# Performance work log

Hardware: AMD Instinct MI355X
Metric: run time of the kernel (lower is better)

The kernel has to match this reference:

```python
import jax, jax.numpy as jnp
import numpy as np

B, LP, LQ, D, H = 4, 256, 256, 256, 256


def setup_inputs() -> dict:
    key = jax.random.key(0)
    ks = jax.random.split(key, 10)
    s_d = 1.0 / np.sqrt(D)
    s_h = 1.0 / np.sqrt(H)
    return {
        "Hp": jax.random.normal(ks[0], (B, LP, D), jnp.float32),
        "Hq": jax.random.normal(ks[1], (B, LQ, D), jnp.float32),
        # weights stored as (in, out); torch Linear does x @ W.T
        "Wc1": jax.random.normal(ks[2], (D, H), jnp.float32) * s_d,
        "Wc2": jax.random.normal(ks[3], (D, H), jnp.float32) * s_d,
        "vc": jax.random.normal(ks[4], (H,), jnp.float32) * s_h,
        "Wb": jax.random.normal(ks[5], (D, D), jnp.float32) * s_d,
        "Wd": jax.random.normal(ks[6], (D, H), jnp.float32) * s_d,
        "vd": jax.random.normal(ks[7], (H,), jnp.float32) * s_h,
        "Wm": jax.random.normal(ks[8], (D, H), jnp.float32) * s_d,
        "vm": jax.random.normal(ks[9], (H,), jnp.float32) * s_h,
    }


def _attend(scores, Hq):
    # scores: (B, Lp, Lq); softmax over Lq then weighted sum of Hq
    a = jax.nn.softmax(scores, axis=2)
    return jnp.einsum("bpq,bqd->bpd", a, Hq)


def reference(Hp, Hq, Wc1, Wc2, vc, Wb, Wd, vd, Wm, vm):
    # branch c: additive attention. tanh(Wc1 Hq + Wc2 Hp) . vc
    s1 = Hq @ Wc1                      # (B, Lq, H)
    s2 = Hp @ Wc2                      # (B, Lp, H)
    sc = jnp.einsum("bpqh,h->bpq", jnp.tanh(s1[:, None, :, :] + s2[:, :, None, :]), vc)
    qc = _attend(sc, Hq)

    # branch b: bilinear attention Hp (Wb Hq)^T
    sb = jnp.einsum("bpd,bqd->bpq", Hp, Hq @ Wb)
    qb = _attend(sb, Hq)

    # branch d: multiplicative interaction. tanh(Wd (Hq * Hp)) . vd
    sd = jnp.einsum("bpqh,h->bpq",
                    jnp.tanh(jnp.einsum("bqk,bpk,kh->bpqh", Hq, Hp, Wd)), vd)
    qd = _attend(sd, Hq)

    # branch m: subtractive interaction. tanh(Wm (Hq - Hp)) . vm
    m1 = Hq @ Wm                       # (B, Lq, H)
    m2 = Hp @ Wm                       # (B, Lp, H)
    sm = jnp.einsum("bpqh,h->bpq", jnp.tanh(m1[:, None, :, :] - m2[:, :, None, :]), vm)
    qm = _attend(sm, Hq)

    return (qc, qb, qd, qm)
```

## Files before the change

kernel.cpp:

```cpp
#include <hip/hip_runtime.h>

#define LOG2E 1.4426950408889634f
#define TANH_S 2.8853900817779268f
#define NB 4
#define NL 256
#define ND 256
#define NH 256

typedef __attribute__((ext_vector_type(8))) short s16x8;
typedef __attribute__((ext_vector_type(4))) short s16x4;
typedef __attribute__((ext_vector_type(4))) float f32x4;
typedef __attribute__((ext_vector_type(2))) unsigned int u32x2;

static __device__ __forceinline__ float b2f(unsigned short u) {
  return __builtin_bit_cast(float, (unsigned int)u << 16);
}
static __device__ __forceinline__ unsigned short f2b(float f) {
  unsigned int x = __builtin_bit_cast(unsigned int, f);
  return (unsigned short)((x + 0x7fffu + ((x >> 16) & 1u)) >> 16);
}
static __device__ __forceinline__ unsigned int cvtpk(float lo, float hi) {
  unsigned int r;
  asm("v_cvt_pk_bf16_f32 %0, %1, %2" : "=v"(r) : "v"(lo), "v"(hi));
  return r;
}


__global__ void __launch_bounds__(256) prep(
    const float* __restrict__ Hq, const float* __restrict__ Hp,
    const float* __restrict__ Wc1, const float* __restrict__ Wc2,
    const float* __restrict__ Wb, const float* __restrict__ Wm,
    const float* __restrict__ Wd, float* __restrict__ ws)
{
  const int which = blockIdx.y;
  const int tid = threadIdx.x;
  __shared__ __align__(16) float a_s[8][256];
  if (which == 5) {
    const int m0 = blockIdx.x * 8;
    unsigned short* AF = (unsigned short*)((char*)ws + 3145728);
    const int row = m0 + (tid >> 5);
    const int grp = tid & 31;
    const int kt = grp >> 2, quad = grp & 3;
    const int k0 = kt * 32 + quad * 8;
    const int bb = row >> 8, q = row & 255;
    const int w = q >> 6, mt = (q >> 4) & 3, c16 = q & 15;
    const float* src = Hq + row * ND + k0;
    f32x4 v0 = *(const f32x4*)(src);
    f32x4 v1 = *(const f32x4*)(src + 4);
    s16x8 o;
    #pragma unroll
    for (int j = 0; j < 4; ++j) { o[j] = (short)f2b(v0[j]); o[4 + j] = (short)f2b(v1[j]); }
    *(s16x8*)(AF + ((((bb * 4 + w) * 4 + mt) * 8 + kt) * 64 + quad * 16 + c16) * 8) = o;
    return;
  }
  if (which == 6) {
    if (blockIdx.x >= 32) return;
    const int k0 = blockIdx.x * 8;
    #pragma unroll
    for (int kk = 0; kk < 8; ++kk)
      a_s[kk][tid] = Wd[(k0 + kk) * NH + tid] * TANH_S;
    __syncthreads();
    float* WdT = (float*)((char*)ws + 4718592);
    f32x4 v0 = {a_s[0][tid], a_s[1][tid], a_s[2][tid], a_s[3][tid]};
    f32x4 v1 = {a_s[4][tid], a_s[5][tid], a_s[6][tid], a_s[7][tid]};
    *(f32x4*)(WdT + tid * 256 + k0) = v0;
    *(f32x4*)(WdT + tid * 256 + k0 + 4) = v1;
    return;
  }
  const int m0 = blockIdx.x * 8;
  const float* A = (which >= 3) ? Hp : Hq;
  const float* W = (which == 0) ? Wc1 : (which == 1) ? Wm :
                   (which == 2) ? Wb  : (which == 3) ? Wc2 : Wm;
  #pragma unroll
  for (int j = 0; j < 8; ++j)
    a_s[j][tid] = A[(m0 + j) * ND + tid];
  __syncthreads();
  float acc[8] = {0.f, 0.f, 0.f, 0.f, 0.f, 0.f, 0.f, 0.f};
  for (int k = 0; k < 256; ++k) {
    const float w = W[k * NH + tid];
    #pragma unroll
    for (int j = 0; j < 8; ++j) acc[j] += a_s[j][k] * w;
  }
  if (which == 2) {
    #pragma unroll
    for (int j = 0; j < 8; ++j) ws[(m0 + j) * NH + tid] = acc[j];
  } else if (which < 2) {
    unsigned short* O = (unsigned short*)((char*)ws + 1048576 + which * 524288);
    #pragma unroll
    for (int j = 0; j < 8; ++j) O[(m0 + j) * NH + tid] = f2b(acc[j] * TANH_S);
  } else {
    unsigned short* O = (unsigned short*)((char*)ws + 2097152 + (which - 3) * 524288);
    #pragma unroll
    for (int j = 0; j < 8; ++j) O[(m0 + j) * NH + tid] = f2b(acc[j] * TANH_S);
  }
}

__global__ void __launch_bounds__(256) dfused(
    const float* __restrict__ Hp, const float* __restrict__ Hq,
    const float* __restrict__ vd, const float* __restrict__ vc,
    const float* __restrict__ vm, const float* __restrict__ ws,
    float* __restrict__ out)
{
  const int p = blockIdx.x, b = blockIdx.y;
  const int tid = threadIdx.x;
  const int wave = tid >> 6, lane = tid & 63;
  const int quad = lane >> 4, c16 = lane & 15;

  __shared__ __align__(16) char ovl[33792];
  __shared__ __align__(16) float sc4[4 * 256];
  __shared__ __align__(16) float hp_s[256];
  __shared__ __align__(16) float invsum[4];

  short* Bs = (short*)ovl;
  float* vd2_s = (float*)(ovl + 32768);
  float* redp = (float*)ovl;
  float* c2_s = (float*)(ovl + 16384);
  float* m2_s = (float*)(ovl + 17408);
  float* vc2_s = (float*)(ovl + 18432);
  float* vm2_s = (float*)(ovl + 19456);

  const unsigned short* AF = (const unsigned short*)((const char*)ws + 3145728);
  const float* WdT = (const float*)((const char*)ws + 4718592);
  const float* X = ws;
  const unsigned short* C1  = (const unsigned short*)((const char*)ws + 1048576);
  const unsigned short* M1  = (const unsigned short*)((const char*)ws + 1572864);
  const unsigned short* C2b = (const unsigned short*)((const char*)ws + 2097152);
  const unsigned short* M2b = (const unsigned short*)((const char*)ws + 2621440);

  hp_s[tid] = Hp[(b * NL + p) * ND + tid];
  vd2_s[tid] = 2.0f * vd[tid];
  __syncthreads();

  {
    const int scol = (tid & 63) * 4;
    const f32x4 hpv = *(const f32x4*)(hp_s + scol);
    const int wq0 = wave * 64;
    const unsigned short* AFw = AF + (b * 4 + wave) * 4 * 8 * 64 * 8;
    const int xswz = (c16 & 7) * 16;

    float sdp[4][4];
    #pragma unroll
    for (int mt = 0; mt < 4; ++mt)
      #pragma unroll
      for (int r = 0; r < 4; ++r) sdp[mt][r] = 0.f;
    float vs2 = 0.f;

    for (int ht = 0; ht < 4; ++ht) {
      const int h0 = ht * 64;
      __syncthreads();
      {
        const float* wsrc = WdT + h0 * 256 + tid * 4;
        #pragma unroll
        for (int i = 0; i < 16; ++i) {
          f32x4 wv = *(const f32x4*)(wsrc + i * 1024);
          const int h = i * 4 + (tid >> 6);
          const unsigned int u0 = cvtpk(wv[0] * hpv[0], wv[1] * hpv[1]);
          const unsigned int u1 = cvtpk(wv[2] * hpv[2], wv[3] * hpv[3]);
          const int baddr = h * 512 + (((tid & 63) * 8) ^ ((h & 7) * 16));
          *(u32x2*)((char*)Bs + baddr) = u32x2{u0, u1};
        }
      }
      __syncthreads();

      f32x4 acc[4][4];
      #pragma unroll
      for (int mt = 0; mt < 4; ++mt)
        #pragma unroll
        for (int nt = 0; nt < 4; ++nt) acc[mt][nt] = f32x4{0.f, 0.f, 0.f, 0.f};

      #pragma unroll 2
      for (int kt = 0; kt < 8; ++kt) {
        s16x8 a8[4];
        #pragma unroll
        for (int mt = 0; mt < 4; ++mt)
          a8[mt] = *(const s16x8*)(AFw + ((mt * 8 + kt) * 64 + lane) * 8);
        #pragma unroll
        for (int nt = 0; nt < 4; ++nt) {
          const int baddr = (nt * 16 + c16) * 512 + ((kt * 64 + quad * 16) ^ xswz);
          s16x8 b8 = *(const s16x8*)((const char*)Bs + baddr);
          #pragma unroll
          for (int mt = 0; mt < 4; ++mt)
            acc[mt][nt] = __builtin_amdgcn_mfma_f32_16x16x32_bf16(
                a8[mt], b8, acc[mt][nt], 0, 0, 0);
        }
      }

      #pragma unroll
      for (int nt = 0; nt < 4; ++nt) {
        const float v2 = vd2_s[h0 + nt * 16 + c16];
        vs2 += v2;
        #pragma unroll
        for (int mt = 0; mt < 4; ++mt) {
          #pragma unroll
          for (int r = 0; r < 4; ++r) {
            float e = __builtin_amdgcn_exp2f(acc[mt][nt][r]);
            sdp[mt][r] += v2 * __builtin_amdgcn_rcpf(e + 1.0f);
          }
        }
      }
    }

    #pragma unroll
    for (int m = 1; m < 16; m <<= 1) vs2 += __shfl_xor(vs2, m, 64);
    #pragma unroll
    for (int mt = 0; mt < 4; ++mt)
      #pragma unroll
      for (int r = 0; r < 4; ++r) {
        float v = sdp[mt][r];
        #pragma unroll
        for (int m = 1; m < 16; m <<= 1) v += __shfl_xor(v, m, 64);
        if (c16 == 0)
          sc4[512 + wq0 + mt * 16 + quad * 4 + r] = 0.5f * vs2 - v;
      }
  }
  __syncthreads();

  {
    const int r = (b * NL + p) * ND + tid;
    c2_s[tid] = b2f(C2b[r]);
    m2_s[tid] = b2f(M2b[r]);
    vc2_s[tid] = 2.0f * vc[tid];
    vm2_s[tid] = 2.0f * vm[tid];
  }
  __syncthreads();

  {
    const int qsub = lane >> 4;
    const int hb = c16 * 4;
    float lc = 0.f, lm = 0.f;
    #pragma unroll
    for (int hi = 0; hi < 4; ++hi) {
      const int h = hb + hi * 64;
      #pragma unroll
      for (int i = 0; i < 4; ++i) { lc += vc2_s[h + i]; lm += vm2_s[h + i]; }
    }
    #pragma unroll
    for (int m = 1; m < 16; m <<= 1) {
      lc += __shfl_xor(lc, m, 64);
      lm += __shfl_xor(lm, m, 64);
    }
    const float c0 = 0.5f * lc, m0 = 0.5f * lm;

    for (int qg = 0; qg < 16; ++qg) {
      const int q = wave * 64 + qg * 4 + qsub;
      const unsigned short* c1r = C1 + (b * NL + q) * NH;
      const unsigned short* m1r = M1 + (b * NL + q) * NH;
      const float* xr = X + (b * NL + q) * ND;
      float pcr0 = 0.f, pmr0 = 0.f, pb0 = 0.f;
      float pcr1 = 0.f, pmr1 = 0.f, pb1 = 0.f;
      #pragma unroll
      for (int hi = 0; hi < 4; ++hi) {
        const int h = hb + hi * 64;
        s16x4 c1v = *(const s16x4*)(c1r + h);
        s16x4 m1v = *(const s16x4*)(m1r + h);
        f32x4 xv  = *(const f32x4*)(xr + h);
        #pragma unroll
        for (int i = 0; i < 4; ++i) {
          float ec = __builtin_amdgcn_exp2f(b2f((unsigned short)c1v[i]) + c2_s[h + i]);
          float em = __builtin_amdgcn_exp2f(b2f((unsigned short)m1v[i]) - m2_s[h + i]);
          if (i & 1) {
            pcr1 += vc2_s[h + i] * __builtin_amdgcn_rcpf(ec + 1.0f);
            pmr1 += vm2_s[h + i] * __builtin_amdgcn_rcpf(em + 1.0f);
            pb1 += hp_s[h + i] * xv[i];
          } else {
            pcr0 += vc2_s[h + i] * __builtin_amdgcn_rcpf(ec + 1.0f);
            pmr0 += vm2_s[h + i] * __builtin_amdgcn_rcpf(em + 1.0f);
            pb0 += hp_s[h + i] * xv[i];
          }
        }
      }
      float pcr = pcr0 + pcr1, pmr = pmr0 + pmr1, pb = pb0 + pb1;
      #pragma unroll
      for (int m = 1; m < 16; m <<= 1) {
        pcr += __shfl_xor(pcr, m, 64);
        pmr += __shfl_xor(pmr, m, 64);
        pb  += __shfl_xor(pb, m, 64);
      }
      if (c16 == 0) {
        sc4[q]       = c0 - pcr;
        sc4[256 + q] = pb;
        sc4[768 + q] = m0 - pmr;
      }
    }
  }
  __syncthreads();

  {
    float s0 = sc4[wave * 256 + lane];
    float s1 = sc4[wave * 256 + lane + 64];
    float s2 = sc4[wave * 256 + lane + 128];
    float s3 = sc4[wave * 256 + lane + 192];
    float mx = fmaxf(fmaxf(s0, s1), fmaxf(s2, s3));
    #pragma unroll
    for (int m = 1; m < 64; m <<= 1) mx = fmaxf(mx, __shfl_xor(mx, m, 64));
    float e0 = __builtin_amdgcn_exp2f((s0 - mx) * LOG2E);
    float e1 = __builtin_amdgcn_exp2f((s1 - mx) * LOG2E);
    float e2 = __builtin_amdgcn_exp2f((s2 - mx) * LOG2E);
    float e3 = __builtin_amdgcn_exp2f((s3 - mx) * LOG2E);
    float sm = e0 + e1 + e2 + e3;
    #pragma unroll
    for (int m = 1; m < 64; m <<= 1) sm += __shfl_xor(sm, m, 64);
    sc4[wave * 256 + lane]       = e0;
    sc4[wave * 256 + lane + 64]  = e1;
    sc4[wave * 256 + lane + 128] = e2;
    sc4[wave * 256 + lane + 192] = e3;
    if (lane == 0) invsum[wave] = __builtin_amdgcn_rcpf(sm);
  }
  __syncthreads();

  {
    const int q0 = wave * 64;
    f32x4 pa0 = {0.f,0.f,0.f,0.f}, pa1 = {0.f,0.f,0.f,0.f};
    f32x4 pa2 = {0.f,0.f,0.f,0.f}, pa3 = {0.f,0.f,0.f,0.f};
    for (int qi = 0; qi < 64; ++qi) {
      const int q = q0 + qi;
      const float ac = sc4[q];
      const float ab = sc4[256 + q];
      const float ad = sc4[512 + q];
      const float am = sc4[768 + q];
      f32x4 hv = *(const f32x4*)(Hq + (b * NL + q) * ND + lane * 4);
      pa0 += ac * hv; pa1 += ab * hv; pa2 += ad * hv; pa3 += am * hv;
    }
    *(f32x4*)(redp + (wave * 4 + 0) * 256 + lane * 4) = pa0;
    *(f32x4*)(redp + (wave * 4 + 1) * 256 + lane * 4) = pa1;
    *(f32x4*)(redp + (wave * 4 + 2) * 256 + lane * 4) = pa2;
    *(f32x4*)(redp + (wave * 4 + 3) * 256 + lane * 4) = pa3;
  }
  __syncthreads();

  {
    #pragma unroll
    for (int br = 0; br < 4; ++br) {
      float s = redp[(0 * 4 + br) * 256 + tid] + redp[(1 * 4 + br) * 256 + tid]
              + redp[(2 * 4 + br) * 256 + tid] + redp[(3 * 4 + br) * 256 + tid];
      out[((br * NB + b) * NL + p) * ND + tid] = s * invsum[br];
    }
  }
}

extern "C" void kernel_launch(void* const* d_in, const int* in_sizes, int n_in,
                              void* d_out, int out_size, void* d_ws, size_t ws_size,
                              hipStream_t stream) {
  const float* Hp  = (const float*)d_in[0];
  const float* Hq  = (const float*)d_in[1];
  const float* Wc1 = (const float*)d_in[2];
  const float* Wc2 = (const float*)d_in[3];
  const float* vc  = (const float*)d_in[4];
  const float* Wb  = (const float*)d_in[5];
  const float* Wd  = (const float*)d_in[6];
  const float* vd  = (const float*)d_in[7];
  const float* Wm  = (const float*)d_in[8];
  const float* vm  = (const float*)d_in[9];
  float* ws = (float*)d_ws;
  float* out = (float*)d_out;

  hipLaunchKernelGGL(prep, dim3(128, 7), dim3(256), 0, stream,
                     Hq, Hp, Wc1, Wc2, Wb, Wm, Wd, ws);
  hipLaunchKernelGGL(dfused, dim3(256, 4), dim3(256), 0, stream,
                     Hp, Hq, vd, vc, vm, ws, out);
}
```

Before: 198.5 us.

## Move projection GEMMs to split-bf16 MFMA kernel with pre-transposed weights

```diff
diff --git a/kernel.cpp b/kernel.cpp
--- a/kernel.cpp
+++ b/kernel.cpp
@@ -27,7 +27,7 @@
 
 
 __global__ void __launch_bounds__(256) prep(
-    const float* __restrict__ Hq, const float* __restrict__ Hp,
+    const float* __restrict__ Hq,
     const float* __restrict__ Wc1, const float* __restrict__ Wc2,
     const float* __restrict__ Wb, const float* __restrict__ Wm,
     const float* __restrict__ Wd, float* __restrict__ ws)
@@ -35,7 +35,7 @@
   const int which = blockIdx.y;
   const int tid = threadIdx.x;
   __shared__ __align__(16) float a_s[8][256];
-  if (which == 5) {
+  if (which == 0) {
     const int m0 = blockIdx.x * 8;
     unsigned short* AF = (unsigned short*)((char*)ws + 3145728);
     const int row = m0 + (tid >> 5);
@@ -53,7 +53,7 @@
     *(s16x8*)(AF + ((((bb * 4 + w) * 4 + mt) * 8 + kt) * 64 + quad * 16 + c16) * 8) = o;
     return;
   }
-  if (which == 6) {
+  if (which == 1) {
     if (blockIdx.x >= 32) return;
     const int k0 = blockIdx.x * 8;
     #pragma unroll
@@ -67,31 +67,95 @@
     *(f32x4*)(WdT + tid * 256 + k0 + 4) = v1;
     return;
   }
-  const int m0 = blockIdx.x * 8;
-  const float* A = (which >= 3) ? Hp : Hq;
-  const float* W = (which == 0) ? Wc1 : (which == 1) ? Wm :
-                   (which == 2) ? Wb  : (which == 3) ? Wc2 : Wm;
+  const int w = blockIdx.x >> 5;
+  const int k0 = (blockIdx.x & 31) * 8;
+  const float* W = (w == 0) ? Wc1 : (w == 1) ? Wm : (w == 2) ? Wb : Wc2;
+  const float scale = (w == 2) ? 1.0f : TANH_S;
   #pragma unroll
-  for (int j = 0; j < 8; ++j)
-    a_s[j][tid] = A[(m0 + j) * ND + tid];
-  __syncthreads();
-  float acc[8] = {0.f, 0.f, 0.f, 0.f, 0.f, 0.f, 0.f, 0.f};
-  for (int k = 0; k < 256; ++k) {
-    const float w = W[k * NH + tid];
-    #pragma unroll
-    for (int j = 0; j < 8; ++j) acc[j] += a_s[j][k] * w;
-  }
-  if (which == 2) {
-    #pragma unroll
-    for (int j = 0; j < 8; ++j) ws[(m0 + j) * NH + tid] = acc[j];
-  } else if (which < 2) {
-    unsigned short* O = (unsigned short*)((char*)ws + 1048576 + which * 524288);
-    #pragma unroll
-    for (int j = 0; j < 8; ++j) O[(m0 + j) * NH + tid] = f2b(acc[j] * TANH_S);
-  } else {
-    unsigned short* O = (unsigned short*)((char*)ws + 2097152 + (which - 3) * 524288);
-    #pragma unroll
-    for (int j = 0; j < 8; ++j) O[(m0 + j) * NH + tid] = f2b(acc[j] * TANH_S);
+  for (int kk = 0; kk < 8; ++kk)
+    a_s[kk][tid] = W[(k0 + kk) * NH + tid] * scale;
+  __syncthreads();
+  unsigned short* WT = (unsigned short*)((char*)ws + 3670016) + w * 131072;
+  s16x8 hi, lo;
+  #pragma unroll
+  for (int kk = 0; kk < 8; ++kk) {
+    float v = a_s[kk][tid];
+    unsigned short h = f2b(v);
+    hi[kk] = (short)h;
+    lo[kk] = (short)f2b(v - b2f(h));
+  }
+  *(s16x8*)(WT + tid * 256 + k0) = hi;
+  *(s16x8*)(WT + 65536 + tid * 256 + k0) = lo;
+}
+
+__global__ void __launch_bounds__(256) gemm5(
+    const float* __restrict__ Hq, const float* __restrict__ Hp,
+    float* __restrict__ ws)
+{
+  const int which = blockIdx.y;
+  const int tid = threadIdx.x;
+  const int wave = tid >> 6, lane = tid & 63;
+  const int quad = lane >> 4, c16 = lane & 15;
+  const int row = blockIdx.x * 64 + wave * 16 + c16;
+
+  const float* A = which ? Hp : Hq;
+  s16x8 ah[8], al[8];
+  #pragma unroll
+  for (int kt = 0; kt < 8; ++kt) {
+    const float* src = A + row * ND + kt * 32 + quad * 8;
+    f32x4 v0 = *(const f32x4*)(src);
+    f32x4 v1 = *(const f32x4*)(src + 4);
+    #pragma unroll
+    for (int j = 0; j < 4; ++j) {
+      unsigned short h0 = f2b(v0[j]);
+      ah[kt][j] = (short)h0;
+      al[kt][j] = (short)f2b(v0[j] - b2f(h0));
+      unsigned short h1 = f2b(v1[j]);
+      ah[kt][4 + j] = (short)h1;
+      al[kt][4 + j] = (short)f2b(v1[j] - b2f(h1));
+    }
+  }
+
+  const unsigned short* WTbase = (const unsigned short*)((const char*)ws + 3670016);
+  const int nmat = which ? 2 : 3;
+  const int orow0 = blockIdx.x * 64 + wave * 16 + quad * 4;
+
+  for (int mi = 0; mi < nmat; ++mi) {
+    const int w = which ? (mi == 0 ? 3 : 1) : mi;
+    const unsigned short* WH = WTbase + w * 131072;
+    const unsigned short* WL = WH + 65536;
+
+    f32x4 acc[16];
+    #pragma unroll
+    for (int nt = 0; nt < 16; ++nt) acc[nt] = f32x4{0.f, 0.f, 0.f, 0.f};
+
+    for (int kt = 0; kt < 8; ++kt) {
+      #pragma unroll
+      for (int nt = 0; nt < 16; ++nt) {
+        const int off = (nt * 16 + c16) * 256 + kt * 32 + quad * 8;
+        s16x8 bh = *(const s16x8*)(WH + off);
+        s16x8 bl = *(const s16x8*)(WL + off);
+        acc[nt] = __builtin_amdgcn_mfma_f32_16x16x32_bf16(ah[kt], bh, acc[nt], 0, 0, 0);
+        acc[nt] = __builtin_amdgcn_mfma_f32_16x16x32_bf16(al[kt], bh, acc[nt], 0, 0, 0);
+        acc[nt] = __builtin_amdgcn_mfma_f32_16x16x32_bf16(ah[kt], bl, acc[nt], 0, 0, 0);
+      }
+    }
+
+    if (w == 2) {
+      #pragma unroll
+      for (int nt = 0; nt < 16; ++nt)
+        #pragma unroll
+        for (int r = 0; r < 4; ++r)
+          ws[(orow0 + r) * NH + nt * 16 + c16] = acc[nt][r];
+    } else {
+      unsigned short* O = (unsigned short*)((char*)ws +
+          (w == 0 ? 1048576 : (w == 1 ? (which ? 2621440 : 1572864) : 2097152)));
+      #pragma unroll
+      for (int nt = 0; nt < 16; ++nt)
+        #pragma unroll
+        for (int r = 0; r < 4; ++r)
+          O[(orow0 + r) * NH + nt * 16 + c16] = f2b(acc[nt][r]);
+    }
   }
 }
 
@@ -354,8 +418,10 @@
   float* ws = (float*)d_ws;
   float* out = (float*)d_out;
 
-  hipLaunchKernelGGL(prep, dim3(128, 7), dim3(256), 0, stream,
-                     Hq, Hp, Wc1, Wc2, Wb, Wm, Wd, ws);
+  hipLaunchKernelGGL(prep, dim3(128, 3), dim3(256), 0, stream,
+                     Hq, Wc1, Wc2, Wb, Wm, Wd, ws);
+  hipLaunchKernelGGL(gemm5, dim3(16, 2), dim3(256), 0, stream,
+                     Hq, Hp, ws);
   hipLaunchKernelGGL(dfused, dim3(256, 4), dim3(256), 0, stream,
                      Hp, Hq, vd, vc, vm, ws, out);
 }
```

Result: slower. 530.0 us (+167.0%).
